# Kernel tuning notes

Hardware: AMD Instinct MI355X
Metric: run time of the kernel (lower is better)

Reference implementation:

```python
import jax, jax.numpy as jnp
import numpy as np

EPS_ATTN = 1e-5   # LinearCrossAttention eps
EPS_LN = 1e-5     # LayerNorm default eps


def _rot_interleaved(t):
    # rotate_half=False path of timm apply_rot_embed_cat: interleaved pairs
    t1 = t[..., ::2]
    t2 = t[..., 1::2]
    return jnp.stack([-t2, t1], axis=-1).reshape(t.shape)


def _apply_rope_cat(t, rope):
    # rope: [N_r, 2*D] = concat(sin, cos); t: [B, H, N_r, D]
    sin, cos = jnp.split(rope, 2, axis=-1)  # each [N_r, D]
    return t * cos + _rot_interleaved(t) * sin


def _layer_norm(x, g, b):
    m = jnp.mean(x, axis=-1, keepdims=True)
    v = jnp.var(x, axis=-1, keepdims=True)
    return (x - m) * jax.lax.rsqrt(v + EPS_LN) * g + b


def setup_inputs() -> dict:
    key = jax.random.key(0)
    ks = jax.random.split(key, 4)
    B, N, C = 8, 4096, 768
    H, D = 12, 64
    npt = 1
    x = jax.random.normal(ks[0], (B, N, C), dtype=jnp.float32)
    rope = jax.random.normal(ks[1], (N - npt, 2 * D), dtype=jnp.float32)
    qkv_w = jax.random.normal(ks[2], (3 * C, C), dtype=jnp.float32) * (C ** -0.5)
    proj_w = jax.random.normal(ks[3], (C, C), dtype=jnp.float32) * (C ** -0.5)
    return {
        "x": x,
        "rope": rope,
        "qkv_w": qkv_w,
        "q_bias": jnp.zeros((C,), jnp.float32),
        "v_bias": jnp.zeros((C,), jnp.float32),
        "norm_g": jnp.ones((C,), jnp.float32),
        "norm_b": jnp.zeros((C,), jnp.float32),
        "proj_w": proj_w,
        "proj_b": jnp.zeros((C,), jnp.float32),
        "num_heads": 12,
        "num_prefix_tokens": 1,
    }


def reference(x, rope, qkv_w, q_bias, v_bias, norm_g, norm_b, proj_w, proj_b,
              num_heads, num_prefix_tokens):
    B, N, C = x.shape
    H = num_heads
    D = C // H
    npt = num_prefix_tokens

    # fused qkv projection; k_bias is a zero buffer
    qkv_bias = jnp.concatenate([q_bias, jnp.zeros_like(q_bias), v_bias])
    qkv = x @ qkv_w.T + qkv_bias                      # [B, N, 3C]
    qkv = qkv.reshape(B, N, 3, H, D).transpose(2, 0, 3, 1, 4)  # [3, B, H, N, D]
    q, k, v = qkv[0], qkv[1], qkv[2]

    # RoPE on non-prefix tokens
    q = jnp.concatenate([q[:, :, :npt], _apply_rope_cat(q[:, :, npt:], rope)], axis=2)
    k = jnp.concatenate([k[:, :, :npt], _apply_rope_cat(k[:, :, npt:], rope)], axis=2)

    # linear cross-attention with tied softmax feature map
    phi_q = jax.nn.softmax(q, axis=-1)                # [B, H, N, D]
    phi_k = jax.nn.softmax(k, axis=-1)                # [B, H, N, D]
    kv = jnp.einsum('bhnd,bhne->bhde', phi_k, v)      # [B, H, D, D]
    z = jnp.einsum('bhnd,bhd->bhn', phi_q, phi_k.sum(axis=2))  # [B, H, N]
    out = jnp.einsum('bhnd,bhde->bhne', phi_q, kv) / (z[..., None] + EPS_ATTN)

    out = out.transpose(0, 2, 1, 3).reshape(B, N, C)  # [B, N, C]
    out = _layer_norm(out, norm_g, norm_b)            # scale_norm
    out = out @ proj_w.T + proj_b
    return out
```

## Files before the change

### kernel.cpp

```cpp
#include <hip/hip_runtime.h>
#include <stdint.h>


typedef __attribute__((ext_vector_type(8))) short short8;
typedef __attribute__((ext_vector_type(4))) float floatx4;

#define SPLIT_A 16
#define TILES_PER_BLK (32 / SPLIT_A)

#define SBAR()  do { asm volatile("" ::: "memory"); __builtin_amdgcn_s_barrier(); asm volatile("" ::: "memory"); } while (0)
#define LGKM0() do { asm volatile("s_waitcnt lgkmcnt(0)" ::: "memory"); __builtin_amdgcn_sched_barrier(0); } while (0)
#define WAITV6() asm volatile("s_waitcnt vmcnt(6)" ::: "memory")
#define WAITV0() asm volatile("s_waitcnt vmcnt(0)" ::: "memory")

__device__ __forceinline__ float b2f(unsigned short u) {
  union { unsigned int i; float f; } v; v.i = ((unsigned int)u) << 16; return v.f;
}
__device__ __forceinline__ unsigned short f2b(float f) {
  union { float f; unsigned int i; } v; v.f = f;
  unsigned int i = v.i;
  unsigned int r = (i + 0x7FFFu + ((i >> 16) & 1u)) >> 16;
  return (unsigned short)r;
}
__device__ __forceinline__ void unpack2(unsigned int u, float& a, float& b) {
  union { unsigned int i; float f; } x, y;
  x.i = u << 16; y.i = u & 0xFFFF0000u;
  a = x.f; b = y.f;
}

__device__ __forceinline__ void stage16(const void* g, void* l) {
#if defined(__has_builtin) && __has_builtin(__builtin_amdgcn_global_load_lds)
  __builtin_amdgcn_global_load_lds(
      (const __attribute__((address_space(1))) unsigned int*)g,
      (__attribute__((address_space(3))) unsigned int*)l, 16, 0, 0);
#else
  *(uint4*)l = *(const uint4*)g;
#endif
}

__global__ __launch_bounds__(256) void f32_to_bf16(
    const float* __restrict__ in, unsigned short* __restrict__ out, int n) {
  const int i = (blockIdx.x * 256 + threadIdx.x) * 8;
  if (i + 7 < n) {
    float4 a = *(const float4*)(in + i);
    float4 b = *(const float4*)(in + i + 4);
    unsigned short tmp[8] = {f2b(a.x), f2b(a.y), f2b(a.z), f2b(a.w),
                             f2b(b.x), f2b(b.y), f2b(b.z), f2b(b.w)};
    *(uint4*)(out + i) = *(uint4*)tmp;
  }
}

__global__ __launch_bounds__(256) void prep(
    const float* __restrict__ w, const float* __restrict__ pw,
    const float* __restrict__ qb, const float* __restrict__ vb,
    const float* __restrict__ pb,
    unsigned short* __restrict__ wbf, unsigned short* __restrict__ pwbf,
    float* __restrict__ qkvb, float* __restrict__ projb) {
  const int blk = blockIdx.x, t = threadIdx.x;
  if (blk < 1152) {
    const float* src = (blk < 864) ? w : pw;
    unsigned short* dst = (blk < 864) ? wbf : pwbf;
    const int i = ((blk < 864 ? blk : blk - 864) * 256 + t) * 8;
    float4 a = *(const float4*)(src + i);
    float4 b = *(const float4*)(src + i + 4);
    unsigned short tmp[8] = {f2b(a.x), f2b(a.y), f2b(a.z), f2b(a.w),
                             f2b(b.x), f2b(b.y), f2b(b.z), f2b(b.w)};
    *(uint4*)(dst + i) = *(uint4*)tmp;
  } else {
    const int i = (blk - 1152) * 256 + t;
    if (i < 2304) qkvb[i] = (i < 768) ? qb[i] : (i >= 1536 ? vb[i - 1536] : 0.f);
    if (i < 768) projb[i] = pb[i];
  }
}

__global__ __launch_bounds__(512, 2) void gemm256(
    const unsigned short* __restrict__ A, const unsigned short* __restrict__ W,
    const float* __restrict__ bias, unsigned short* __restrict__ Out,
    int K, int Nout, int nbn, int NT) {
  extern __shared__ __align__(16) unsigned short lds[];
  const int nwg = gridDim.x;
  const int orig = blockIdx.x;
  const int wg = (orig & 7) * (nwg >> 3) + (orig >> 3);
  const int bm = wg / nbn, bn = wg - bm * nbn;
  const int t = threadIdx.x;
  const int lane = t & 63, wave = t >> 6;
  const int wr = wave >> 2, wc = wave & 3;
  const int mr = lane & 15, kq8 = lane >> 4;

  const int rh0 = t >> 3, sl0 = t & 7;
  const size_t growA = (size_t)bm * 256;
  const size_t growB = (size_t)bn * 256;

  #define STAGE_HALF(buf, op, G, grow, k0, half)                               \
    do {                                                                       \
      const int row0_ = (half)*128 + rh0;                                      \
      const int row1_ = row0_ + 64;                                            \
      const unsigned short* s0_ =                                              \
          (G) + ((grow) + row0_) * (size_t)K + (k0) + ((sl0 ^ (row0_ & 7)) * 8);\
      const unsigned short* s1_ =                                              \
          (G) + ((grow) + row1_) * (size_t)K + (k0) + ((sl0 ^ (row1_ & 7)) * 8);\
      unsigned short* d0_ = lds + (buf)*32768 + (op)*16384 + (half)*8192 + t*8;\
      stage16(s0_, d0_);                                                       \
      stage16(s1_, d0_ + 4096);                                                \
    } while (0)

  floatx4 acc[8][4] = {};
  short8 afr[4][2], bfr[4][2];

  #define RD_A(buf, i, kk)                                                     \
    (*(const short8*)&lds[(buf)*32768 + (wr*128 + (i)*16 + mr)*64 +            \
        ((((kk)*4 + kq8) ^ ((wr*128 + (i)*16 + mr) & 7)) * 8)])
  #define RD_B(buf, j, kk)                                                     \
    (*(const short8*)&lds[(buf)*32768 + 16384 + (wc*64 + (j)*16 + mr)*64 +     \
        ((((kk)*4 + kq8) ^ ((wc*64 + (j)*16 + mr) & 7)) * 8)])

  #define QUAD(ih, jh)                                                         \
    do {                                                                       \
      __builtin_amdgcn_s_setprio(1);                                           \
      _Pragma("unroll")                                                        \
      for (int i_ = 0; i_ < 4; i_++)                                           \
        _Pragma("unroll")                                                      \
        for (int jr_ = 0; jr_ < 2; jr_++)                                      \
          _Pragma("unroll")                                                    \
          for (int kk_ = 0; kk_ < 2; kk_++)                                    \
            acc[(ih)*4 + i_][(jh)*2 + jr_] =                                   \
                __builtin_amdgcn_mfma_f32_16x16x32_bf16(                       \
                    bfr[(jh)*2 + jr_][kk_], afr[i_][kk_],                      \
                    acc[(ih)*4 + i_][(jh)*2 + jr_], 0, 0, 0);                  \
      __builtin_amdgcn_s_setprio(0);                                           \
    } while (0)

  STAGE_HALF(0, 0, A, growA, 0, 0);
  STAGE_HALF(0, 0, A, growA, 0, 1);
  STAGE_HALF(0, 1, W, growB, 0, 0);
  STAGE_HALF(0, 1, W, growB, 0, 1);
  STAGE_HALF(1, 1, W, growB, 64, 0);
  STAGE_HALF(1, 1, W, growB, 64, 1);
  STAGE_HALF(1, 0, A, growA, 64, 0);
  WAITV6();
  SBAR();

  const int NI = NT >> 1;
  for (int it = 0; it < NI; ++it) {
    const int ta = 2 * it, tb = ta + 1;
    const int kA = (ta + 2) * 64, kB = (tb + 2) * 64;
    const bool gA = (ta + 2) < NT, gB = (tb + 2) < NT;
#pragma unroll
    for (int i = 0; i < 4; i++) { afr[i][0] = RD_A(0, i, 0); afr[i][1] = RD_A(0, i, 1); }
#pragma unroll
    for (int j = 0; j < 4; j++) { bfr[j][0] = RD_B(0, j, 0); bfr[j][1] = RD_B(0, j, 1); }
    STAGE_HALF(1, 0, A, growA, tb * 64, 1);
    SBAR(); LGKM0();
    QUAD(0, 0);
    SBAR();
    if (gA) STAGE_HALF(0, 1, W, growB, kA, 0);
    SBAR();
    QUAD(0, 1);
    SBAR();
#pragma unroll
    for (int i = 0; i < 4; i++) { afr[i][0] = RD_A(0, i + 4, 0); afr[i][1] = RD_A(0, i + 4, 1); }
    if (gA) STAGE_HALF(0, 1, W, growB, kA, 1);
    SBAR(); LGKM0();
    QUAD(1, 0);
    SBAR();
    if (gA) STAGE_HALF(0, 0, A, growA, kA, 0);
    SBAR();
    QUAD(1, 1);
    if (gA) WAITV6(); else WAITV0();
    SBAR();
#pragma unroll
    for (int i = 0; i < 4; i++) { afr[i][0] = RD_A(1, i, 0); afr[i][1] = RD_A(1, i, 1); }
#pragma unroll
    for (int j = 0; j < 4; j++) { bfr[j][0] = RD_B(1, j, 0); bfr[j][1] = RD_B(1, j, 1); }
    if (gA) STAGE_HALF(0, 0, A, growA, kA, 1);
    SBAR(); LGKM0();
    QUAD(0, 0);
    SBAR();
    if (gB) STAGE_HALF(1, 1, W, growB, kB, 0);
    SBAR();
    QUAD(0, 1);
    SBAR();
#pragma unroll
    for (int i = 0; i < 4; i++) { afr[i][0] = RD_A(1, i + 4, 0); afr[i][1] = RD_A(1, i + 4, 1); }
    if (gB) STAGE_HALF(1, 1, W, growB, kB, 1);
    SBAR(); LGKM0();
    QUAD(1, 0);
    SBAR();
    if (gB) STAGE_HALF(1, 0, A, growA, kB, 0);
    SBAR();
    QUAD(1, 1);
    if (gB) WAITV6(); else WAITV0();
    SBAR();
  }

  const int fr = lane & 15, fq4 = (lane >> 4) * 4;
#pragma unroll
  for (int i = 0; i < 8; i++) {
    const int lrow = wr * 128 + i * 16 + fr;
#pragma unroll
    for (int j = 0; j < 4; j++) {
      const int colu = wc * 64 + j * 16 + fq4;
      const float4 bv = *(const float4*)&bias[bn * 256 + colu];
      unsigned short pk[4] = {f2b(acc[i][j][0] + bv.x), f2b(acc[i][j][1] + bv.y),
                              f2b(acc[i][j][2] + bv.z), f2b(acc[i][j][3] + bv.w)};
      const int chunk = colu >> 3;
      const int low = colu & 7;
      *(uint2*)&lds[lrow * 256 + ((chunk ^ (lrow & 7)) << 3) + low] =
          *(const uint2*)pk;
    }
  }
  SBAR();
#pragma unroll
  for (int p = 0; p < 16; p++) {
    const int row = p * 16 + (t >> 5);
    const int chunk = t & 31;
    uint4 v = *(const uint4*)&lds[row * 256 + ((chunk ^ (row & 7)) << 3)];
    *(uint4*)(Out + (size_t)(bm * 256 + row) * Nout + bn * 256 + chunk * 8) = v;
  }
  #undef STAGE_HALF
  #undef RD_A
  #undef RD_B
  #undef QUAD
}

template <int OUT_BF16>
__global__ __launch_bounds__(256) void gemm_bt(
    const unsigned short* __restrict__ A, const unsigned short* __restrict__ W,
    const float* __restrict__ bias, void* __restrict__ Out,
    int M, int K, int Nout, int nbn) {
  __shared__ __align__(16) unsigned short sA[128 * 32];
  __shared__ __align__(16) unsigned short sB[128 * 32];
  const int nwg = gridDim.x;
  const int orig = blockIdx.x;
  const int wg = (orig & 7) * (nwg >> 3) + (orig >> 3);
  const int bm = wg / nbn;
  const int bn = wg - bm * nbn;
  const int t = threadIdx.x;
  const int lane = t & 63, wave = t >> 6;
  const int wm = (wave >> 1) * 64, wn = (wave & 1) * 64;
  const int lr = t >> 2;
  const int lc = (t & 3) * 8;
  const size_t baseA = (size_t)(bm * 128 + lr) * K + lc;
  const size_t baseB = (size_t)(bn * 128 + lr) * K + lc;
  floatx4 acc[4][4] = {};

  const int mr = lane & 15, kq = (lane >> 4) * 8;
  for (int k0 = 0; k0 < K; k0 += 32) {
    stage16(A + baseA + k0, &sA[t * 8]);
    stage16(A + baseA + (size_t)64 * K + k0, &sA[2048 + t * 8]);
    stage16(W + baseB + k0, &sB[t * 8]);
    stage16(W + baseB + (size_t)64 * K + k0, &sB[2048 + t * 8]);
    __syncthreads();
    short8 af[4], bfr[4];
#pragma unroll
    for (int i = 0; i < 4; i++) af[i] = *(const short8*)&sA[(wm + i * 16 + mr) * 32 + kq];
#pragma unroll
    for (int j = 0; j < 4; j++) bfr[j] = *(const short8*)&sB[(wn + j * 16 + mr) * 32 + kq];
#pragma unroll
    for (int i = 0; i < 4; i++)
#pragma unroll
      for (int j = 0; j < 4; j++)
        acc[i][j] = __builtin_amdgcn_mfma_f32_16x16x32_bf16(af[i], bfr[j], acc[i][j], 0, 0, 0);
    __syncthreads();
  }

  const int mr4 = (lane >> 4) * 4, nc = lane & 15;
#pragma unroll
  for (int j = 0; j < 4; j++) {
    const int gc = bn * 128 + wn + j * 16 + nc;
    const float bv = bias[gc];
#pragma unroll
    for (int i = 0; i < 4; i++) {
      const int gr0 = bm * 128 + wm + i * 16 + mr4;
#pragma unroll
      for (int r = 0; r < 4; r++) {
        float v = acc[i][j][r] + bv;
        if (OUT_BF16)
          ((unsigned short*)Out)[(size_t)(gr0 + r) * Nout + gc] = f2b(v);
        else
          ((float*)Out)[(size_t)(gr0 + r) * Nout + gc] = v;
      }
    }
  }
}

__global__ __launch_bounds__(256) void pass_a(
    const unsigned short* __restrict__ qkv, const float* __restrict__ rope,
    float* __restrict__ kvP) {
  __shared__ float sphi[128 * 65];
  __shared__ __align__(16) unsigned short sv[128 * 64];
  const int bh = blockIdx.x, b = bh / 12, h = bh % 12;
  const int sp = blockIdx.y;
  const int t = threadIdx.x;
  const int lane = t & 63, wave = t >> 6;
  const int dg = lane >> 2;
  const int eg = lane & 3;
  float acc[4][16] = {};
  float ks4[4] = {};

  const int tile0 = sp * TILES_PER_BLK;
  for (int tile = tile0; tile < tile0 + TILES_PER_BLK; tile++) {
    __syncthreads();
    if (t < 128) {
      const int n = tile * 128 + t;
      const size_t rowb = (size_t)(b * 4096 + n) * 2304;
      const unsigned short* kp = qkv + rowb + 768 + h * 64;
      float kk[64];
#pragma unroll
      for (int c = 0; c < 8; c++) {
        uint4 u = *(const uint4*)(kp + c * 8);
        unpack2(u.x, kk[c * 8 + 0], kk[c * 8 + 1]);
        unpack2(u.y, kk[c * 8 + 2], kk[c * 8 + 3]);
        unpack2(u.z, kk[c * 8 + 4], kk[c * 8 + 5]);
        unpack2(u.w, kk[c * 8 + 6], kk[c * 8 + 7]);
      }
      if (n > 0) {
        const float* rp = rope + (size_t)(n - 1) * 128;
#pragma unroll
        for (int c = 0; c < 8; c++) {
          float sn[8], cs[8];
          *(float4*)&sn[0] = *(const float4*)(rp + c * 8);
          *(float4*)&sn[4] = *(const float4*)(rp + c * 8 + 4);
          *(float4*)&cs[0] = *(const float4*)(rp + 64 + c * 8);
          *(float4*)&cs[4] = *(const float4*)(rp + 64 + c * 8 + 4);
#pragma unroll
          for (int i = 0; i < 4; i++) {
            float e = kk[c * 8 + 2 * i], o = kk[c * 8 + 2 * i + 1];
            kk[c * 8 + 2 * i] = e * cs[2 * i] - o * sn[2 * i];
            kk[c * 8 + 2 * i + 1] = o * cs[2 * i + 1] + e * sn[2 * i + 1];
          }
        }
      }
      float mx = kk[0];
#pragma unroll
      for (int i = 1; i < 64; i++) mx = fmaxf(mx, kk[i]);
      float s = 0.f;
#pragma unroll
      for (int i = 0; i < 64; i++) { float e = __expf(kk[i] - mx); kk[i] = e; s += e; }
      const float inv = 1.f / s;
#pragma unroll
      for (int d = 0; d < 64; d++) sphi[t * 65 + d] = kk[d] * inv;
      const unsigned short* vp = qkv + rowb + 1536 + h * 64;
#pragma unroll
      for (int c = 0; c < 8; c++)
        *(uint4*)&sv[t * 64 + c * 8] = *(const uint4*)(vp + c * 8);
    }
    __syncthreads();
    const int n0 = wave * 32;
    for (int nn = n0; nn < n0 + 32; nn++) {
      float p[4];
#pragma unroll
      for (int i = 0; i < 4; i++) p[i] = sphi[nn * 65 + dg * 4 + i];
#pragma unroll
      for (int i = 0; i < 4; i++) ks4[i] += p[i];
      float vv[16];
      {
        uint4 u0 = *(const uint4*)&sv[nn * 64 + eg * 16];
        uint4 u1 = *(const uint4*)&sv[nn * 64 + eg * 16 + 8];
        unpack2(u0.x, vv[0], vv[1]);   unpack2(u0.y, vv[2], vv[3]);
        unpack2(u0.z, vv[4], vv[5]);   unpack2(u0.w, vv[6], vv[7]);
        unpack2(u1.x, vv[8], vv[9]);   unpack2(u1.y, vv[10], vv[11]);
        unpack2(u1.z, vv[12], vv[13]); unpack2(u1.w, vv[14], vv[15]);
      }
#pragma unroll
      for (int i = 0; i < 4; i++)
#pragma unroll
        for (int j = 0; j < 16; j++)
          acc[i][j] += p[i] * vv[j];
    }
  }

  __syncthreads();
  float* sred = sphi;
  float* o = kvP + ((size_t)bh * SPLIT_A + sp) * 4160;
#pragma unroll
  for (int half = 0; half < 2; half++) {
    if (wave != 0) {
      float* row = &sred[((wave - 1) * 64 + lane) * 33];
#pragma unroll
      for (int i = 0; i < 4; i++)
#pragma unroll
        for (int jj = 0; jj < 8; jj++) row[i * 8 + jj] = acc[i][half * 8 + jj];
    }
    __syncthreads();
    if (wave == 0) {
#pragma unroll
      for (int jj = 0; jj < 8; jj++) {
        float4 s4;
        float sv4[4];
#pragma unroll
        for (int i = 0; i < 4; i++) {
          float s = acc[i][half * 8 + jj];
#pragma unroll
          for (int w = 0; w < 3; w++) s += sred[(w * 64 + lane) * 33 + i * 8 + jj];
          sv4[i] = s;
        }
        s4.x = sv4[0]; s4.y = sv4[1]; s4.z = sv4[2]; s4.w = sv4[3];
        const int e = eg * 16 + half * 8 + jj;
        *(float4*)&o[e * 64 + dg * 4] = s4;
      }
    }
    __syncthreads();
  }
  if (wave != 0) {
#pragma unroll
    for (int i = 0; i < 4; i++) sred[((wave - 1) * 64 + lane) * 5 + i] = ks4[i];
  }
  __syncthreads();
  if (wave == 0 && eg == 0) {
    float4 s4;
    float sv4[4];
#pragma unroll
    for (int i = 0; i < 4; i++) {
      float s = ks4[i];
#pragma unroll
      for (int w = 0; w < 3; w++) s += sred[(w * 64 + lane) * 5 + i];
      sv4[i] = s;
    }
    s4.x = sv4[0]; s4.y = sv4[1]; s4.z = sv4[2]; s4.w = sv4[3];
    *(float4*)&o[4096 + dg * 4] = s4;
  }
}

__global__ __launch_bounds__(256) void reduce_kv(
    const float* __restrict__ kvP, float* __restrict__ kvG) {
  const int i = blockIdx.x * 256 + threadIdx.x;
  if (i >= 96 * 4160) return;
  const int bh = i / 4160, r = i - bh * 4160;
  const float* p = kvP + (size_t)bh * SPLIT_A * 4160 + r;
  float s = 0.f;
#pragma unroll
  for (int sp = 0; sp < SPLIT_A; sp++) s += p[(size_t)sp * 4160];
  kvG[i] = s;
}

__global__ __launch_bounds__(256) void pass_b(
    const unsigned short* __restrict__ qkv, const float* __restrict__ rope,
    const float* __restrict__ kvG, unsigned short* __restrict__ attn) {
  __shared__ __align__(16) unsigned short sp_[256 * 64];
  __shared__ __align__(16) unsigned short skv[64 * 64];
  __shared__ float szi[256];
  __shared__ float sks[64];
  const int bh = blockIdx.x, b = bh / 12, h = bh % 12;
  const int t = threadIdx.x;
  const float* kvb = kvG + (size_t)bh * 4160;

  {
    const int e = t >> 2, q = t & 3;
    const float* src = kvb + e * 64 + q * 16;
    unsigned short tmp[16];
#pragma unroll
    for (int i = 0; i < 16; i++) tmp[i] = f2b(src[i]);
    *(uint4*)&skv[e * 64 + (((q * 2) ^ (e & 7)) * 8)] = *(uint4*)&tmp[0];
    *(uint4*)&skv[e * 64 + (((q * 2 + 1) ^ (e & 7)) * 8)] = *(uint4*)&tmp[8];
  }
  if (t < 64) sks[t] = kvb[4096 + t];
  __syncthreads();

  const int n = blockIdx.y * 256 + t;
  const size_t rowb = (size_t)(b * 4096 + n) * 2304;
  const unsigned short* qp = qkv + rowb + h * 64;
  float ph[64];
#pragma unroll
  for (int c = 0; c < 8; c++) {
    uint4 u = *(const uint4*)(qp + c * 8);
    unpack2(u.x, ph[c * 8 + 0], ph[c * 8 + 1]);
    unpack2(u.y, ph[c * 8 + 2], ph[c * 8 + 3]);
    unpack2(u.z, ph[c * 8 + 4], ph[c * 8 + 5]);
    unpack2(u.w, ph[c * 8 + 6], ph[c * 8 + 7]);
  }
  if (n > 0) {
    const float* rp = rope + (size_t)(n - 1) * 128;
#pragma unroll
    for (int c = 0; c < 8; c++) {
      float sn[8], cs[8];
      *(float4*)&sn[0] = *(const float4*)(rp + c * 8);
      *(float4*)&sn[4] = *(const float4*)(rp + c * 8 + 4);
      *(float4*)&cs[0] = *(const float4*)(rp + 64 + c * 8);
      *(float4*)&cs[4] = *(const float4*)(rp + 64 + c * 8 + 4);
#pragma unroll
      for (int i = 0; i < 4; i++) {
        float e = ph[c * 8 + 2 * i], o = ph[c * 8 + 2 * i + 1];
        ph[c * 8 + 2 * i] = e * cs[2 * i] - o * sn[2 * i];
        ph[c * 8 + 2 * i + 1] = o * cs[2 * i + 1] + e * sn[2 * i + 1];
      }
    }
  }
  float mx = ph[0];
#pragma unroll
  for (int i = 1; i < 64; i++) mx = fmaxf(mx, ph[i]);
  float s = 0.f;
#pragma unroll
  for (int i = 0; i < 64; i++) { float e = __expf(ph[i] - mx); ph[i] = e; s += e; }
  const float inv = 1.f / s;
  float z = 0.f;
#pragma unroll
  for (int i = 0; i < 64; i++) { ph[i] *= inv; z += ph[i] * sks[i]; }
  szi[t] = 1.f / (z + 1e-5f);

#pragma unroll
  for (int sl = 0; sl < 8; sl += 2) {
    unsigned short tmp[16];
#pragma unroll
    for (int i = 0; i < 16; i++) tmp[i] = f2b(ph[sl * 8 + i]);
    *(uint4*)&sp_[t * 64 + ((sl ^ (t & 7)) * 8)] = *(uint4*)&tmp[0];
    *(uint4*)&sp_[t * 64 + (((sl + 1) ^ (t & 7)) * 8)] = *(uint4*)&tmp[8];
  }
  __syncthreads();

  const int lane = t & 63, wv = t >> 6;
  const int fr = lane & 15, fq = lane >> 4;
  floatx4 acc[4][4] = {};
#pragma unroll
  for (int kk = 0; kk < 2; kk++) {
    short8 kvf[4], pf[4];
#pragma unroll
    for (int j = 0; j < 4; j++) {
      const int e = j * 16 + fr;
      kvf[j] = *(const short8*)&skv[e * 64 + (((kk * 4 + fq) ^ (e & 7)) * 8)];
    }
#pragma unroll
    for (int i = 0; i < 4; i++) {
      const int tok = wv * 64 + i * 16 + fr;
      pf[i] = *(const short8*)&sp_[tok * 64 + (((kk * 4 + fq) ^ (tok & 7)) * 8)];
    }
#pragma unroll
    for (int i = 0; i < 4; i++)
#pragma unroll
      for (int j = 0; j < 4; j++)
        acc[i][j] = __builtin_amdgcn_mfma_f32_16x16x32_bf16(kvf[j], pf[i], acc[i][j], 0, 0, 0);
  }

#pragma unroll
  for (int i = 0; i < 4; i++) {
    const int tokl = wv * 64 + i * 16 + fr;
    const float zi = szi[tokl];
    unsigned short* orow =
        attn + (size_t)(b * 4096 + blockIdx.y * 256 + tokl) * 768 + h * 64;
#pragma unroll
    for (int j = 0; j < 4; j++) {
      const int e0 = j * 16 + fq * 4;
      unsigned short pk[4] = {f2b(acc[i][j][0] * zi), f2b(acc[i][j][1] * zi),
                              f2b(acc[i][j][2] * zi), f2b(acc[i][j][3] * zi)};
      *(uint2*)(orow + e0) = *(const uint2*)pk;
    }
  }
}

__global__ __launch_bounds__(256) void ln_kernel(
    unsigned short* __restrict__ buf, const float* __restrict__ g,
    const float* __restrict__ be) {
  const int row = blockIdx.x;
  const int t = threadIdx.x;
  unsigned short* p = buf + (size_t)row * 768;
  const float x0 = b2f(p[t]), x1 = b2f(p[t + 256]), x2 = b2f(p[t + 512]);
  float s = x0 + x1 + x2;
  float ss = x0 * x0 + x1 * x1 + x2 * x2;
#pragma unroll
  for (int m = 1; m < 64; m <<= 1) { s += __shfl_xor(s, m); ss += __shfl_xor(ss, m); }
  __shared__ float red[8];
  const int wave = t >> 6, lane = t & 63;
  if (lane == 0) { red[wave] = s; red[4 + wave] = ss; }
  __syncthreads();
  s = red[0] + red[1] + red[2] + red[3];
  ss = red[4] + red[5] + red[6] + red[7];
  const float mean = s * (1.f / 768.f);
  const float var = ss * (1.f / 768.f) - mean * mean;
  const float rsq = rsqrtf(var + 1e-5f);
  p[t] = f2b((x0 - mean) * rsq * g[t] + be[t]);
  p[t + 256] = f2b((x1 - mean) * rsq * g[t + 256] + be[t + 256]);
  p[t + 512] = f2b((x2 - mean) * rsq * g[t + 512] + be[t + 512]);
}

extern "C" void kernel_launch(void* const* d_in, const int* in_sizes, int n_in,
                              void* d_out, int out_size, void* d_ws, size_t ws_size,
                              hipStream_t stream) {
  (void)in_sizes; (void)n_in; (void)out_size; (void)ws_size;
  const float* x      = (const float*)d_in[0];
  const float* rope   = (const float*)d_in[1];
  const float* qkv_w  = (const float*)d_in[2];
  const float* q_bias = (const float*)d_in[3];
  const float* v_bias = (const float*)d_in[4];
  const float* norm_g = (const float*)d_in[5];
  const float* norm_b = (const float*)d_in[6];
  const float* proj_w = (const float*)d_in[7];
  const float* proj_b = (const float*)d_in[8];

  char* ws = (char*)d_ws;
  unsigned short* qkv  = (unsigned short*)ws;
  unsigned short* attn = (unsigned short*)(ws + 150994944);
  unsigned short* xbf  = attn;
  float* kvP   = (float*)(ws + 150994944);
  float* kvG   = (float*)(ws + 201326592);
  float* qkvb  = (float*)(ws + 202924032);
  float* projb = (float*)(ws + 202933248);
  unsigned short* wbf  = (unsigned short*)(ws + 202936320);
  unsigned short* pwbf = (unsigned short*)(ws + 206475264);

  hipFuncSetAttribute(reinterpret_cast<const void*>(&gemm256),
                      hipFuncAttributeMaxDynamicSharedMemorySize, 131072);

  f32_to_bf16<<<dim3(12288), dim3(256), 0, stream>>>(x, xbf, 25165824);
  prep<<<dim3(1161), dim3(256), 0, stream>>>(qkv_w, proj_w, q_bias, v_bias,
                                             proj_b, wbf, pwbf, qkvb, projb);
  gemm256<<<dim3(1152), dim3(512), 131072, stream>>>(xbf, wbf, qkvb, qkv,
                                                     768, 2304, 9, 12);
  pass_a<<<dim3(96, SPLIT_A), dim3(256), 0, stream>>>(qkv, rope, kvP);
  reduce_kv<<<dim3(1560), dim3(256), 0, stream>>>(kvP, kvG);
  pass_b<<<dim3(96, 16), dim3(256), 0, stream>>>(qkv, rope, kvG, attn);
  ln_kernel<<<dim3(32768), dim3(256), 0, stream>>>(attn, norm_g, norm_b);
  gemm_bt<0><<<dim3(1536), dim3(256), 0, stream>>>(attn, pwbf, projb, d_out,
                                                   32768, 768, 768, 6);
}
```

Before: 562.1 us.

## Compute pass_a phi_k^T V partials with bf16 MFMA over swizzled transposed LDS

pass_a used to build phi_k and V for each 256-token chunk in two tiles of 128, then form the 64x64 kv outer-product sum with scalar FMAs on fp32 LDS data and reduce across waves. Now all 256 threads each compute one token's RoPE and softmax. The results are written as bf16 into XOR-swizzled transposed LDS buffers, and the kv and k-sum partials come from 16x16x32 bf16 MFMAs, the k-sum by multiplying against a vector of ones. This removes the scalar FMA loop and the cross-wave LDS reduction. The cost is that phi_k is rounded to bf16 before accumulation, which may change accuracy slightly.

```diff
diff --git a/kernel.cpp b/kernel.cpp
--- a/kernel.cpp
+++ b/kernel.cpp
@@ -6,7 +6,6 @@
 typedef __attribute__((ext_vector_type(4))) float floatx4;
 
 #define SPLIT_A 16
-#define TILES_PER_BLK (32 / SPLIT_A)
 
 #define SBAR()  do { asm volatile("" ::: "memory"); __builtin_amdgcn_s_barrier(); asm volatile("" ::: "memory"); } while (0)
 #define LGKM0() do { asm volatile("s_waitcnt lgkmcnt(0)" ::: "memory"); __builtin_amdgcn_sched_barrier(0); } while (0)
@@ -287,138 +286,100 @@
 __global__ __launch_bounds__(256) void pass_a(
     const unsigned short* __restrict__ qkv, const float* __restrict__ rope,
     float* __restrict__ kvP) {
-  __shared__ float sphi[128 * 65];
-  __shared__ __align__(16) unsigned short sv[128 * 64];
+  __shared__ __align__(16) unsigned short sphiT[64 * 256];
+  __shared__ __align__(16) unsigned short svT[64 * 256];
   const int bh = blockIdx.x, b = bh / 12, h = bh % 12;
   const int sp = blockIdx.y;
   const int t = threadIdx.x;
-  const int lane = t & 63, wave = t >> 6;
-  const int dg = lane >> 2;
-  const int eg = lane & 3;
-  float acc[4][16] = {};
-  float ks4[4] = {};
-
-  const int tile0 = sp * TILES_PER_BLK;
-  for (int tile = tile0; tile < tile0 + TILES_PER_BLK; tile++) {
-    __syncthreads();
-    if (t < 128) {
-      const int n = tile * 128 + t;
-      const size_t rowb = (size_t)(b * 4096 + n) * 2304;
-      const unsigned short* kp = qkv + rowb + 768 + h * 64;
-      float kk[64];
-#pragma unroll
-      for (int c = 0; c < 8; c++) {
-        uint4 u = *(const uint4*)(kp + c * 8);
-        unpack2(u.x, kk[c * 8 + 0], kk[c * 8 + 1]);
-        unpack2(u.y, kk[c * 8 + 2], kk[c * 8 + 3]);
-        unpack2(u.z, kk[c * 8 + 4], kk[c * 8 + 5]);
-        unpack2(u.w, kk[c * 8 + 6], kk[c * 8 + 7]);
+
+  const int n = sp * 256 + t;
+  const size_t rowb = (size_t)(b * 4096 + n) * 2304;
+  const unsigned short* kp = qkv + rowb + 768 + h * 64;
+  float kk[64];
+#pragma unroll
+  for (int c = 0; c < 8; c++) {
+    uint4 u = *(const uint4*)(kp + c * 8);
+    unpack2(u.x, kk[c * 8 + 0], kk[c * 8 + 1]);
+    unpack2(u.y, kk[c * 8 + 2], kk[c * 8 + 3]);
+    unpack2(u.z, kk[c * 8 + 4], kk[c * 8 + 5]);
+    unpack2(u.w, kk[c * 8 + 6], kk[c * 8 + 7]);
+  }
+  if (n > 0) {
+    const float* rp = rope + (size_t)(n - 1) * 128;
+#pragma unroll
+    for (int c = 0; c < 8; c++) {
+      float sn[8], cs[8];
+      *(float4*)&sn[0] = *(const float4*)(rp + c * 8);
+      *(float4*)&sn[4] = *(const float4*)(rp + c * 8 + 4);
+      *(float4*)&cs[0] = *(const float4*)(rp + 64 + c * 8);
+      *(float4*)&cs[4] = *(const float4*)(rp + 64 + c * 8 + 4);
+#pragma unroll
+      for (int i = 0; i < 4; i++) {
+        float e = kk[c * 8 + 2 * i], o = kk[c * 8 + 2 * i + 1];
+        kk[c * 8 + 2 * i] = e * cs[2 * i] - o * sn[2 * i];
+        kk[c * 8 + 2 * i + 1] = o * cs[2 * i + 1] + e * sn[2 * i + 1];
       }
-      if (n > 0) {
-        const float* rp = rope + (size_t)(n - 1) * 128;
-#pragma unroll
-        for (int c = 0; c < 8; c++) {
-          float sn[8], cs[8];
-          *(float4*)&sn[0] = *(const float4*)(rp + c * 8);
-          *(float4*)&sn[4] = *(const float4*)(rp + c * 8 + 4);
-          *(float4*)&cs[0] = *(const float4*)(rp + 64 + c * 8);
-          *(float4*)&cs[4] = *(const float4*)(rp + 64 + c * 8 + 4);
-#pragma unroll
-          for (int i = 0; i < 4; i++) {
-            float e = kk[c * 8 + 2 * i], o = kk[c * 8 + 2 * i + 1];
-            kk[c * 8 + 2 * i] = e * cs[2 * i] - o * sn[2 * i];
-            kk[c * 8 + 2 * i + 1] = o * cs[2 * i + 1] + e * sn[2 * i + 1];
-          }
-        }
-      }
-      float mx = kk[0];
-#pragma unroll
-      for (int i = 1; i < 64; i++) mx = fmaxf(mx, kk[i]);
-      float s = 0.f;
-#pragma unroll
-      for (int i = 0; i < 64; i++) { float e = __expf(kk[i] - mx); kk[i] = e; s += e; }
-      const float inv = 1.f / s;
-#pragma unroll
-      for (int d = 0; d < 64; d++) sphi[t * 65 + d] = kk[d] * inv;
-      const unsigned short* vp = qkv + rowb + 1536 + h * 64;
-#pragma unroll
-      for (int c = 0; c < 8; c++)
-        *(uint4*)&sv[t * 64 + c * 8] = *(const uint4*)(vp + c * 8);
-    }
-    __syncthreads();
-    const int n0 = wave * 32;
-    for (int nn = n0; nn < n0 + 32; nn++) {
-      float p[4];
-#pragma unroll
-      for (int i = 0; i < 4; i++) p[i] = sphi[nn * 65 + dg * 4 + i];
-#pragma unroll
-      for (int i = 0; i < 4; i++) ks4[i] += p[i];
-      float vv[16];
-      {
-        uint4 u0 = *(const uint4*)&sv[nn * 64 + eg * 16];
-        uint4 u1 = *(const uint4*)&sv[nn * 64 + eg * 16 + 8];
-        unpack2(u0.x, vv[0], vv[1]);   unpack2(u0.y, vv[2], vv[3]);
-        unpack2(u0.z, vv[4], vv[5]);   unpack2(u0.w, vv[6], vv[7]);
-        unpack2(u1.x, vv[8], vv[9]);   unpack2(u1.y, vv[10], vv[11]);
-        unpack2(u1.z, vv[12], vv[13]); unpack2(u1.w, vv[14], vv[15]);
-      }
-#pragma unroll
-      for (int i = 0; i < 4; i++)
-#pragma unroll
-        for (int j = 0; j < 16; j++)
-          acc[i][j] += p[i] * vv[j];
-    }
-  }
-
+    }
+  }
+  float mx = kk[0];
+#pragma unroll
+  for (int i = 1; i < 64; i++) mx = fmaxf(mx, kk[i]);
+  float s = 0.f;
+#pragma unroll
+  for (int i = 0; i < 64; i++) { float e = __expf(kk[i] - mx); kk[i] = e; s += e; }
+  const float inv = 1.f / s;
+
+  const int tc = t >> 3, tl = t & 7;
+#pragma unroll
+  for (int d = 0; d < 64; d++)
+    sphiT[d * 256 + ((tc ^ (d & 7)) * 8) + tl] = f2b(kk[d] * inv);
+  {
+    const unsigned short* vp = qkv + rowb + 1536 + h * 64;
+    unsigned short vraw[64];
+#pragma unroll
+    for (int c = 0; c < 8; c++)
+      *(uint4*)&vraw[c * 8] = *(const uint4*)(vp + c * 8);
+#pragma unroll
+    for (int e = 0; e < 64; e++)
+      svT[e * 256 + ((tc ^ (e & 7)) * 8) + tl] = vraw[e];
+  }
   __syncthreads();
-  float* sred = sphi;
+
+  const int lane = t & 63, w = t >> 6;
+  const int mr = lane & 15, kq = lane >> 4;
+  floatx4 acc[4] = {};
+  floatx4 accs = {};
+  short8 ones;
+#pragma unroll
+  for (int i = 0; i < 8; i++) ones[i] = (short)0x3F80;
+  const int d = w * 16 + mr;
+#pragma unroll
+  for (int ks = 0; ks < 8; ks++) {
+    const int clog = ks * 4 + kq;
+    short8 af = *(const short8*)&sphiT[d * 256 + ((clog ^ (d & 7)) * 8)];
+#pragma unroll
+    for (int j = 0; j < 4; j++) {
+      const int e = j * 16 + mr;
+      short8 bf_ = *(const short8*)&svT[e * 256 + ((clog ^ (e & 7)) * 8)];
+      acc[j] = __builtin_amdgcn_mfma_f32_16x16x32_bf16(af, bf_, acc[j], 0, 0, 0);
+    }
+    accs = __builtin_amdgcn_mfma_f32_16x16x32_bf16(af, ones, accs, 0, 0, 0);
+  }
+
   float* o = kvP + ((size_t)bh * SPLIT_A + sp) * 4160;
-#pragma unroll
-  for (int half = 0; half < 2; half++) {
-    if (wave != 0) {
-      float* row = &sred[((wave - 1) * 64 + lane) * 33];
-#pragma unroll
-      for (int i = 0; i < 4; i++)
-#pragma unroll
-        for (int jj = 0; jj < 8; jj++) row[i * 8 + jj] = acc[i][half * 8 + jj];
-    }
-    __syncthreads();
-    if (wave == 0) {
-#pragma unroll
-      for (int jj = 0; jj < 8; jj++) {
-        float4 s4;
-        float sv4[4];
-#pragma unroll
-        for (int i = 0; i < 4; i++) {
-          float s = acc[i][half * 8 + jj];
-#pragma unroll
-          for (int w = 0; w < 3; w++) s += sred[(w * 64 + lane) * 33 + i * 8 + jj];
-          sv4[i] = s;
-        }
-        s4.x = sv4[0]; s4.y = sv4[1]; s4.z = sv4[2]; s4.w = sv4[3];
-        const int e = eg * 16 + half * 8 + jj;
-        *(float4*)&o[e * 64 + dg * 4] = s4;
-      }
-    }
-    __syncthreads();
-  }
-  if (wave != 0) {
-#pragma unroll
-    for (int i = 0; i < 4; i++) sred[((wave - 1) * 64 + lane) * 5 + i] = ks4[i];
-  }
-  __syncthreads();
-  if (wave == 0 && eg == 0) {
+  const int dr0 = w * 16 + (lane >> 4) * 4;
+  const int nc = lane & 15;
+#pragma unroll
+  for (int j = 0; j < 4; j++) {
+    const int e = j * 16 + nc;
     float4 s4;
-    float sv4[4];
-#pragma unroll
-    for (int i = 0; i < 4; i++) {
-      float s = ks4[i];
-#pragma unroll
-      for (int w = 0; w < 3; w++) s += sred[(w * 64 + lane) * 5 + i];
-      sv4[i] = s;
-    }
-    s4.x = sv4[0]; s4.y = sv4[1]; s4.z = sv4[2]; s4.w = sv4[3];
-    *(float4*)&o[4096 + dg * 4] = s4;
+    s4.x = acc[j][0]; s4.y = acc[j][1]; s4.z = acc[j][2]; s4.w = acc[j][3];
+    *(float4*)&o[e * 64 + dr0] = s4;
+  }
+  if (nc == 0) {
+    float4 s4;
+    s4.x = accs[0]; s4.y = accs[1]; s4.z = accs[2]; s4.w = accs[3];
+    *(float4*)&o[4096 + dr0] = s4;
   }
 }
 
```

After: 520.5 us. -7.4%, faster.
